# Kernel optimization log

Hardware: AMD Instinct MI355X
Metric: run time of the kernel (lower is better)

Reference implementation:

```python
import jax, jax.numpy as jnp
import numpy as np
from jax import lax

L = 12  # db6 filter length
REC_LO = np.array([0.11154074335008017, 0.4946238903983854, 0.7511339080215775,
                   0.3152503517092432, -0.22626469396516913, -0.12976686756709563,
                   0.09750160558707936, 0.02752286553001629, -0.031582039318031156,
                   0.0005538422009938016, 0.004777257511010651, -0.00107730108499558])
DEC_LO = REC_LO[::-1]
_sgn = (-1.0) ** np.arange(L)
DEC_HI = -_sgn * REC_LO            # pywt dec_hi
REC_HI = _sgn * DEC_LO             # pywt rec_hi
# XLA conv = cross-correlation; pytorch_wavelets correlates with reversed dec filters
K_ANA = np.ascontiguousarray(np.stack([DEC_LO[::-1], DEC_HI[::-1]])[:, None, :])  # (2,1,12)
# conv_transpose(stride2, pad L-2) == dilate-by-2, pad 1, correlate with flipped rec filters
K_SYN = np.ascontiguousarray(np.stack([REC_LO[::-1], REC_HI[::-1]])[None, :, :])  # (1,2,12)
J = 8


def _afb(x):
    # one analysis level, symmetric mode (pytorch_wavelets afb1d)
    B, C, N = x.shape
    out = (N + L - 1) // 2
    p = 2 * (out - 1) - N + L
    xp = jnp.pad(x, ((0, 0), (0, 0), (p // 2, p - p // 2)), mode='symmetric')
    y = lax.conv_general_dilated(xp.reshape(B * C, 1, -1), jnp.asarray(K_ANA, x.dtype),
                                 (2,), 'VALID', dimension_numbers=('NCH', 'OIH', 'NCH'))
    y = y.reshape(B, C, 2, out)
    return y[:, :, 0], y[:, :, 1]


def _sfb(lo, hi):
    # one synthesis level (pytorch_wavelets sfb1d); crop lo to hi length first
    lo = lo[..., :hi.shape[-1]]
    B, C, N = lo.shape
    z = jnp.stack([lo, hi], 2).reshape(B * C, 2, N)
    y = lax.conv_general_dilated(z, jnp.asarray(K_SYN, lo.dtype), (1,), [(1, 1)],
                                 lhs_dilation=(2,), dimension_numbers=('NCH', 'OIH', 'NCH'))
    return y.reshape(B, C, -1)  # length 2N - L + 2


def _wave_conv(x, w1, w2):
    lo, highs = x, []
    for _ in range(J):
        lo, hi = _afb(lo)
        highs.append(hi)
    lo = jnp.einsum('bix,iox->box', lo, w1)
    highs[-1] = jnp.einsum('bix,iox->box', highs[-1], w2)
    for hi in highs[::-1]:
        lo = _sfb(lo, hi)
    return lo


def _branch(xg, fc0_w, fc0_b, ww1, ww2, cw, cb, fc1_w, fc1_b, fc2_w, fc2_b):
    v = jnp.transpose(xg @ fc0_w + fc0_b, (0, 2, 1))  # (B,C,S)
    for i in range(4):
        a = _wave_conv(v, ww1[i], ww2[i])
        b = jnp.einsum('bcs,oc->bos', v, cw[i]) + cb[i][None, :, None]
        v = a + b
        if i < 3:
            v = jax.nn.gelu(v, approximate=False)
    v = jnp.transpose(v, (0, 2, 1))
    v = jax.nn.gelu(v @ fc1_w + fc1_b, approximate=False)
    return v @ fc2_w + fc2_b


def setup_inputs() -> dict:
    key = jax.random.key(0)
    ks = iter(jax.random.split(key, 32))
    B, S, W, LV = 64, 1024, 64, 8
    d = {"x": jax.random.normal(next(ks), (B, S, 1), jnp.float32)}
    def params(pref):
        sc = 1.0 / (W * W)
        d[pref + "fc0_w"] = jax.random.normal(next(ks), (2, W), jnp.float32) * 0.5
        d[pref + "fc0_b"] = jax.random.normal(next(ks), (W,), jnp.float32) * 0.1
        d[pref + "wave_w1"] = sc * jax.random.uniform(next(ks), (4, W, W, LV + 6), jnp.float32)
        d[pref + "wave_w2"] = sc * jax.random.uniform(next(ks), (4, W, W, LV + 6), jnp.float32)
        d[pref + "cw"] = jax.random.normal(next(ks), (4, W, W), jnp.float32) * (1.0 / np.sqrt(W))
        d[pref + "cb"] = jax.random.normal(next(ks), (4, W), jnp.float32) * 0.05
        d[pref + "fc1_w"] = jax.random.normal(next(ks), (W, 128), jnp.float32) * (1.0 / np.sqrt(W))
        d[pref + "fc1_b"] = jax.random.normal(next(ks), (128,), jnp.float32) * 0.05
        d[pref + "fc2_w"] = jax.random.normal(next(ks), (128, 1), jnp.float32) * (1.0 / np.sqrt(128))
        d[pref + "fc2_b"] = jax.random.normal(next(ks), (1,), jnp.float32) * 0.05
    params("")
    params("nt_")
    return d


def reference(x, fc0_w, fc0_b, wave_w1, wave_w2, cw, cb, fc1_w, fc1_b, fc2_w, fc2_b,
              nt_fc0_w, nt_fc0_b, nt_wave_w1, nt_wave_w2, nt_cw, nt_cb,
              nt_fc1_w, nt_fc1_b, nt_fc2_w, nt_fc2_b):
    B, S, _ = x.shape
    grid = jnp.broadcast_to(jnp.linspace(0.0, 1.0, S, dtype=x.dtype)[None, :, None], (B, S, 1))
    xg = jnp.concatenate([x, grid], -1)
    y = _branch(xg, fc0_w, fc0_b, wave_w1, wave_w2, cw, cb, fc1_w, fc1_b, fc2_w, fc2_b)
    y_nt = _branch(xg, nt_fc0_w, nt_fc0_b, nt_wave_w1, nt_wave_w2, nt_cw, nt_cb,
                   nt_fc1_w, nt_fc1_b, nt_fc2_w, nt_fc2_b)
    return y + y_nt
```

## Files before the change

kernel.cpp:

```cpp
#include <hip/hip_runtime.h>
#include <hip/hip_bf16.h>
#include <math.h>


#define BDIM 64
#define SLEN 1024
#define WCH  64
#define BC   (BDIM*WCH)
#define NT   16

typedef short s16x8 __attribute__((ext_vector_type(8)));
typedef float f32x4 __attribute__((ext_vector_type(4)));
typedef unsigned short u16x4 __attribute__((ext_vector_type(4)));

constexpr float RLv[12] = {
    0.11154074335008017f, 0.4946238903983854f, 0.7511339080215775f,
    0.3152503517092432f, -0.22626469396516913f, -0.12976686756709563f,
    0.09750160558707936f, 0.02752286553001629f, -0.031582039318031156f,
    0.0005538422009938016f, 0.004777257511010651f, -0.00107730108499558f };
constexpr float AHv[12] = {
     RLv[11], -RLv[10],  RLv[9], -RLv[8],  RLv[7], -RLv[6],
     RLv[5],  -RLv[4],   RLv[3], -RLv[2],  RLv[1], -RLv[0] };
constexpr float SLv[12] = {
     RLv[11], RLv[10], RLv[9], RLv[8], RLv[7], RLv[6],
     RLv[5],  RLv[4],  RLv[3], RLv[2], RLv[1], RLv[0] };
constexpr float SHv[12] = {
    -RLv[0],  RLv[1], -RLv[2],  RLv[3], -RLv[4],  RLv[5],
    -RLv[6],  RLv[7], -RLv[8],  RLv[9], -RLv[10], RLv[11] };

__device__ __forceinline__ float gelu_f(float x) {
    float z = 0.7978845608f * (x + 0.044715f * x * x * x);
    return x / (1.0f + __expf(-2.0f * z));
}
__device__ __forceinline__ unsigned short f2bf(float f) {
    __hip_bfloat16 h = __float2bfloat16(f);
    union { __hip_bfloat16 h; unsigned short u; } cv; cv.h = h; return cv.u;
}
__device__ __forceinline__ float bf2f(unsigned short u) {
    union { unsigned short u; __hip_bfloat16 h; } cv; cv.u = u;
    return __bfloat162float(cv.h);
}
__device__ __forceinline__ void unpack_frag2(uint4 a, uint4 b,
                                             s16x8* ah, s16x8* al) {
    union { s16x8 v; unsigned int d[4]; } H, L;
    H.d[0] = __builtin_amdgcn_perm(a.y, a.x, 0x05040100u);
    H.d[1] = __builtin_amdgcn_perm(a.w, a.z, 0x05040100u);
    H.d[2] = __builtin_amdgcn_perm(b.y, b.x, 0x05040100u);
    H.d[3] = __builtin_amdgcn_perm(b.w, b.z, 0x05040100u);
    L.d[0] = __builtin_amdgcn_perm(a.y, a.x, 0x07060302u);
    L.d[1] = __builtin_amdgcn_perm(a.w, a.z, 0x07060302u);
    L.d[2] = __builtin_amdgcn_perm(b.y, b.x, 0x07060302u);
    L.d[3] = __builtin_amdgcn_perm(b.w, b.z, 0x07060302u);
    *ah = H.v; *al = L.v;
}

__device__ __forceinline__ int swz(int c, int s) {
    return c * 64 + ((((s >> 3) ^ (c & 7)) << 3) | (s & 7));
}
__device__ __forceinline__ int swz2(int s, int c) {
    return s * 64 + ((((c >> 3) ^ (s & 7)) << 3) | (c & 7));
}

__device__ __forceinline__ void proj2(
    const unsigned short* Phi, const unsigned short* Plo,
    const unsigned short* __restrict__ Ahi, const unsigned short* __restrict__ Alo,
    float* __restrict__ Ppart, int bb, int tile, int s0, int t)
{
    const int lane = t & 63;
    const int w    = t >> 6;
    const int qr   = lane >> 4;
    const int ln   = lane & 15;

    s16x8 pah[2][2], pal[2][2];
#pragma unroll
    for (int kk = 0; kk < 2; ++kk)
#pragma unroll
        for (int mt = 0; mt < 2; ++mt) {
            const int arow = (mt * 16 + ln) * SLEN + s0 + kk * 32 + qr * 8;
            pah[kk][mt] = *(const s16x8*)&Ahi[arow];
            pal[kk][mt] = *(const s16x8*)&Alo[arow];
        }

    f32x4 pP[2][2], pS[2][2];
#pragma unroll
    for (int mt = 0; mt < 2; ++mt)
#pragma unroll
        for (int ni = 0; ni < 2; ++ni) {
            pP[mt][ni] = (f32x4){0.f,0.f,0.f,0.f};
            pS[mt][ni] = (f32x4){0.f,0.f,0.f,0.f};
        }

#pragma unroll
    for (int kk = 0; kk < 2; ++kk) {
        const int bk = kk * 4 + qr;
#pragma unroll
        for (int ni = 0; ni < 2; ++ni) {
            const int c = w * 32 + ni * 16 + ln;
            const int boff = c * 64 + ((bk ^ (c & 7)) << 3);
            s16x8 bh = *(const s16x8*)&Phi[boff];
            s16x8 bl = *(const s16x8*)&Plo[boff];
#pragma unroll
            for (int mt = 0; mt < 2; ++mt) {
                pP[mt][ni] = __builtin_amdgcn_mfma_f32_16x16x32_bf16(pah[kk][mt], bh, pP[mt][ni], 0, 0, 0);
                pS[mt][ni] = __builtin_amdgcn_mfma_f32_16x16x32_bf16(pal[kk][mt], bh, pS[mt][ni], 0, 0, 0);
                pS[mt][ni] = __builtin_amdgcn_mfma_f32_16x16x32_bf16(pah[kk][mt], bl, pS[mt][ni], 0, 0, 0);
            }
        }
    }
#pragma unroll
    for (int mt = 0; mt < 2; ++mt)
#pragma unroll
        for (int ni = 0; ni < 2; ++ni) {
            const int c = w * 32 + ni * 16 + ln;
            f32x4 pv = pP[mt][ni] + pS[mt][ni];
#pragma unroll
            for (int r = 0; r < 4; ++r) {
                const int xr = mt * 16 + qr * 4 + r;
                if (xr < 28)
                    Ppart[((size_t)(bb * NT + tile) * 28 + xr) * 64 + c] = pv[r];
            }
        }
}

__global__ __launch_bounds__(256) void setup_kernel(
    const float* __restrict__ x,
    unsigned short* __restrict__ Ahi, unsigned short* __restrict__ Alo,
    unsigned short* __restrict__ MThi, unsigned short* __restrict__ MTlo,
    float* __restrict__ axbuf,
    const float* __restrict__ fc1w_0, const float* __restrict__ fc1w_1,
    const float* __restrict__ cw_0, const float* __restrict__ cw_1,
    const float* __restrict__ w1_0, const float* __restrict__ w2_0,
    const float* __restrict__ w1_1, const float* __restrict__ w2_1,
    unsigned short* __restrict__ w1hi, unsigned short* __restrict__ w1lo,
    unsigned short* __restrict__ cwPhi, unsigned short* __restrict__ cwPlo,
    unsigned short* __restrict__ Dhi,  unsigned short* __restrict__ Dlo,
    float* __restrict__ WsT)
{
    __shared__ float Af[1024];
    __shared__ float Bff[520];
    __shared__ float hib[14];
    const int t = threadIdx.x;

    if (blockIdx.x < 1024 || (blockIdx.x >= 1052 && blockIdx.x < 1118)) {
        const bool isA = (blockIdx.x < 1024);
        const int s0 = blockIdx.x;
        const int di = blockIdx.x - 1052;
        for (int i = t; i < SLEN; i += 256) {
            float v;
            if (isA)           v = (i == s0) ? 1.0f : 0.0f;
            else if (di < 64)  v = x[di * SLEN + i];
            else if (di == 64) v = (float)i * (1.0f / 1023.0f);
            else               v = 1.0f;
            Af[i] = v;
        }
        __syncthreads();

        const int NIN[8]  = {1024, 517, 264, 137, 74, 42, 26, 18};
        const int NOUT[8] = { 517, 264, 137,  74, 42, 26, 18, 14};
#pragma unroll
        for (int lev = 0; lev < 8; ++lev) {
            float* in  = (lev & 1) ? Bff : Af;
            float* out = (lev & 1) ? Af : Bff;
            const int nin = NIN[lev], nout = NOUT[lev];
            for (int m = t; m < nout; m += 256) {
                float alo = 0.f, ahi = 0.f;
#pragma unroll
                for (int tt = 0; tt < 12; ++tt) {
                    int jj = 2 * m + tt - 10;
                    if (jj < 0)         jj = -1 - jj;
                    else if (jj >= nin) jj = 2 * nin - 1 - jj;
                    float xv = in[jj];
                    alo += xv * RLv[tt];
                    if (lev == 7) ahi += xv * AHv[tt];
                }
                out[m] = alo;
                if (lev == 7) {
                    if (isA) {
                        unsigned short h1 = f2bf(alo);
                        Ahi[m * SLEN + s0] = h1;
                        Alo[m * SLEN + s0] = f2bf(alo - bf2f(h1));
                        unsigned short h2 = f2bf(ahi);
                        Ahi[(14 + m) * SLEN + s0] = h2;
                        Alo[(14 + m) * SLEN + s0] = f2bf(ahi - bf2f(h2));
                    } else {
                        axbuf[di * 28 + m]      = alo;
                        axbuf[di * 28 + 14 + m] = ahi;
                    }
                }
            }
            __syncthreads();
        }
        if (isA && t < 4) {
            Ahi[(28 + t) * SLEN + s0] = 0; Alo[(28 + t) * SLEN + s0] = 0;
            MThi[s0 * 32 + 28 + t] = 0;    MTlo[s0 * 32 + 28 + t] = 0;
        }
        return;
    }

    if (blockIdx.x >= 1126) {
        const int wsb = blockIdx.x - 1126;
        const int L = wsb >> 2, br = (wsb >> 1) & 1, which = wsb & 1;
        const float* src = (which ? (br ? w2_1 : w2_0) : (br ? w1_1 : w1_0))
                         + (size_t)L * 64 * 64 * 14;
        const size_t dbase = ((size_t)(L * 2 + br) * 28 + which * 14) * 4096;
        for (int e = t; e < 4096; e += 256) {
            const float* sp = src + (size_t)e * 14;
            float v[14];
#pragma unroll
            for (int xi = 0; xi < 14; ++xi) v[xi] = sp[xi];
#pragma unroll
            for (int xi = 0; xi < 14; ++xi)
                WsT[dbase + (size_t)xi * 4096 + e] = v[xi];
        }
        return;
    }

    if (blockIdx.x >= 1118) {
        const int gid = (blockIdx.x - 1118) * 256 + t;
        for (int idx = gid; idx < 16384; idx += 2048) {
            int br = idx >> 13, r = idx & 8191;
            int h = r >> 6, c = r & 63;
            float f = (br ? fc1w_1 : fc1w_0)[c * 128 + h];
            unsigned short hh = f2bf(f);
            w1hi[idx] = hh;
            w1lo[idx] = f2bf(f - bf2f(hh));
        }
        for (int idx = gid; idx < 32768; idx += 2048) {
            int L = idx >> 13, br = (idx >> 12) & 1, e = idx & 4095;
            int k = e >> 6, o = e & 63;
            float val = (br ? cw_1 : cw_0)[(size_t)L * 4096 + o * 64 + k]
                      + ((k == o) ? 1.0f : 0.0f);
            unsigned short h = f2bf(val);
            const int off = (L * 2 + br) * 4096 + o * 64 + k;
            cwPhi[off] = h;
            cwPlo[off] = f2bf(val - bf2f(h));
        }
        for (int idx = gid; idx < 32768; idx += 2048) {
            int bb = idx >> 8, o = (idx >> 2) & 63, j = idx & 3;
            Dhi[bb * 2048 + o * 32 + 28 + j] = 0;
            Dlo[bb * 2048 + o * 32 + 28 + j] = 0;
        }
        return;
    }

    const int u = blockIdx.x - 1024;
    if (t < 14) {
        Af[t]  = (u < 14 && t == u) ? 1.0f : 0.0f;
        hib[t] = (u >= 14 && t == (u - 14)) ? 1.0f : 0.0f;
    }
    __syncthreads();

    const int NH[8] = {14, 18, 26, 42, 74, 137, 264, 517};
    const int NO[8] = {18, 26, 42, 74, 138, 264, 518, 1024};

#pragma unroll
    for (int s = 0; s < 8; ++s) {
        const float* lo = (s & 1) ? Bff : Af;
        float* out      = (s & 1) ? Af : Bff;
        const int N = NH[s], nout = NO[s];
        for (int m = t; m < nout; m += 256) {
            float acc = 0.f;
#pragma unroll
            for (int tt = 0; tt < 12; ++tt) {
                int uu = m + tt - 1;
                if ((uu & 1) == 0) {
                    int q = uu >> 1;
                    if (q < N) {
                        acc += lo[q] * SLv[tt];
                        if (s == 0) acc += hib[q] * SHv[tt];
                    }
                }
            }
            out[m] = acc;
        }
        __syncthreads();
    }
    for (int m = t; m < SLEN; m += 256) {
        float f = Af[m];
        unsigned short h = f2bf(f);
        MThi[m * 32 + u] = h;
        MTlo[m * 32 + u] = f2bf(f - bf2f(h));
    }
}

__global__ __launch_bounds__(256) void mix0_kernel(
    const float* __restrict__ axbuf,
    const float* __restrict__ fc0w_0, const float* __restrict__ fc0b_0,
    const float* __restrict__ fc0w_1, const float* __restrict__ fc0b_1,
    const float* __restrict__ WsT0,
    unsigned short* __restrict__ Dhi, unsigned short* __restrict__ Dlo)
{
    const int t = threadIdx.x;
    const int br  = blockIdx.x / 224;
    const int sub = blockIdx.x % 224;

    __shared__ float Ws[64][65];
    __shared__ float LO[8][64];
    const int o = t & 63;
    const int w = t >> 6;
    const int x  = sub >> 3;
    const int b0 = (sub & 7) << 3;

    const float* wsrc = WsT0 + ((size_t)(br * 28 + x)) * 4096;
    for (int idx = t; idx < 4096; idx += 256)
        Ws[idx >> 6][idx & 63] = wsrc[idx];

    const float* fc0w = br ? fc0w_1 : fc0w_0;
    const float* fc0b = br ? fc0b_1 : fc0b_0;
    const float agv = axbuf[64 * 28 + x];
    const float a1v = axbuf[65 * 28 + x];
    const float w0o = fc0w[o];
    const float wgo = fc0w[WCH + o];
    const float b0o = fc0b[o];

#pragma unroll
    for (int j = 0; j < 2; ++j) {
        int bi = w + 4 * j;
        int b  = b0 + bi;
        float axv = axbuf[b * 28 + x];
        LO[bi][o] = axv * w0o + agv * wgo + a1v * b0o;
    }
    __syncthreads();

#pragma unroll
    for (int j = 0; j < 2; ++j) {
        int bi = w + 4 * j;
        int bb = br * 64 + b0 + bi;
        float acc = 0.f;
        for (int i = 0; i < 64; ++i)
            acc += LO[bi][i] * Ws[i][o];
        acc -= LO[bi][o];
        unsigned short h = f2bf(acc);
        Dhi[bb * 2048 + o * 32 + x] = h;
        Dlo[bb * 2048 + o * 32 + x] = f2bf(acc - bf2f(h));
    }
}

__global__ __launch_bounds__(256) void mix_kernel(
    const float* __restrict__ Ppart,
    const float* __restrict__ WsTL,
    unsigned short* __restrict__ Dhi, unsigned short* __restrict__ Dlo)
{
    const int t = threadIdx.x;
    const int br  = blockIdx.x / 224;
    const int sub = blockIdx.x % 224;

    __shared__ float Ws[64][65];
    __shared__ float LO[8][64];
    const int o = t & 63;
    const int w = t >> 6;
    const int x  = sub >> 3;
    const int b0 = (sub & 7) << 3;

    const float* wsrc = WsTL + ((size_t)(br * 28 + x)) * 4096;
    for (int idx = t; idx < 4096; idx += 256)
        Ws[idx >> 6][idx & 63] = wsrc[idx];

#pragma unroll
    for (int j = 0; j < 2; ++j) {
        int bi = w + 4 * j;
        int bb = br * 64 + b0 + bi;
        float s = 0.f;
        for (int tile = 0; tile < NT; ++tile)
            s += Ppart[((size_t)(bb * NT + tile) * 28 + x) * 64 + o];
        LO[bi][o] = s;
    }
    __syncthreads();

#pragma unroll
    for (int j = 0; j < 2; ++j) {
        int bi = w + 4 * j;
        int bb = br * 64 + b0 + bi;
        float acc = 0.f;
        for (int i = 0; i < 64; ++i)
            acc += LO[bi][i] * Ws[i][o];
        acc -= LO[bi][o];
        unsigned short h = f2bf(acc);
        Dhi[bb * 2048 + o * 32 + x] = h;
        Dlo[bb * 2048 + o * 32 + x] = f2bf(acc - bf2f(h));
    }
}

__global__ __launch_bounds__(128, 3) void layer_kernel(
    const unsigned int* __restrict__ vin0, const unsigned int* __restrict__ vin1,
    unsigned int* __restrict__ vout0, unsigned int* __restrict__ vout1,
    const unsigned short* __restrict__ MThi, const unsigned short* __restrict__ MTlo,
    const unsigned short* __restrict__ Ahi,  const unsigned short* __restrict__ Alo,
    const unsigned short* __restrict__ cwPhi, const unsigned short* __restrict__ cwPlo,
    const unsigned short* __restrict__ Dhi,   const unsigned short* __restrict__ Dlo,
    const float* __restrict__ cb_0, const float* __restrict__ cb_1,
    const float* __restrict__ fc0w_0, const float* __restrict__ fc0b_0,
    const float* __restrict__ fc0w_1, const float* __restrict__ fc0b_1,
    const float* __restrict__ xin,
    float* __restrict__ Ppart, int Lidx)
{
    __shared__ unsigned short Phi[4096];
    __shared__ unsigned short Plo[4096];

    const int t = threadIdx.x;
    const int bid = blockIdx.x;
    const int br  = bid >> 10;
    const int rem = bid & 1023;
    const int b    = rem >> 4;
    const int tile = rem & 15;
    const int s0   = tile << 6;
    const size_t bS = (size_t)b * SLEN;
    const unsigned int* vin = br ? vin1 : vin0;
    unsigned int* vout      = br ? vout1 : vout0;
    const float* cb = br ? cb_1 : cb_0;
    const float* f0w = br ? fc0w_1 : fc0w_0;
    const float* f0b = br ? fc0b_1 : fc0b_0;
    const int bb = br * 64 + b;
    const int cwbase = (Lidx * 2 + br) * 4096;

    const int lane = t & 63;
    const int w    = t >> 6;
    const int qr   = lane >> 4;
    const int ln   = lane & 15;

    s16x8 Bh[2][2], Bl[2][2];
#pragma unroll
    for (int kk = 0; kk < 2; ++kk)
#pragma unroll
        for (int ni = 0; ni < 2; ++ni) {
            const int o = w * 32 + ni * 16 + ln;
            const int boff = cwbase + o * 64 + kk * 32 + qr * 8;
            Bh[kk][ni] = *(const s16x8*)&cwPhi[boff];
            Bl[kk][ni] = *(const s16x8*)&cwPlo[boff];
        }
    s16x8 Dhf[2], Dlf[2];
#pragma unroll
    for (int ni = 0; ni < 2; ++ni) {
        const int o = w * 32 + ni * 16 + ln;
        const int boff = bb * 2048 + o * 32 + qr * 8;
        Dhf[ni] = *(const s16x8*)&Dhi[boff];
        Dlf[ni] = *(const s16x8*)&Dlo[boff];
    }
    float cbv[2];
#pragma unroll
    for (int ni = 0; ni < 2; ++ni) cbv[ni] = cb[w * 32 + ni * 16 + ln];

    uint4 vb[2][2];
    float xpf = 0.f;
    if (Lidx == 0) {
        xpf = xin[bS + s0 + ln];
    } else {
        const size_t a0 = (bS + s0 + ln) * 64 + qr * 8;
        vb[0][0] = *(const uint4*)&vin[a0];
        vb[0][1] = *(const uint4*)&vin[a0 + 4];
        vb[1][0] = *(const uint4*)&vin[a0 + 32];
        vb[1][1] = *(const uint4*)&vin[a0 + 36];
    }

#pragma unroll
    for (int mi = 0; mi < 4; ++mi) {
        const int srow = mi * 16 + ln;
        uint4 vn[2][2];
        float xnf = 0.f;
        if (mi < 3) {
            if (Lidx == 0) {
                xnf = xin[bS + s0 + (mi + 1) * 16 + ln];
            } else {
                const size_t an = (bS + s0 + (mi + 1) * 16 + ln) * 64 + qr * 8;
                vn[0][0] = *(const uint4*)&vin[an];
                vn[0][1] = *(const uint4*)&vin[an + 4];
                vn[1][0] = *(const uint4*)&vin[an + 32];
                vn[1][1] = *(const uint4*)&vin[an + 36];
            }
        }

        f32x4 accP[2], accS[2];
#pragma unroll
        for (int ni = 0; ni < 2; ++ni) {
            accP[ni] = (f32x4){0.f,0.f,0.f,0.f};
            accS[ni] = (f32x4){0.f,0.f,0.f,0.f};
        }

#pragma unroll
        for (int kk = 0; kk < 2; ++kk) {
            s16x8 ah, al;
            if (Lidx == 0) {
                const int s = s0 + srow;
                const float gv = (float)s * (1.0f / 1023.0f);
#pragma unroll
                for (int j = 0; j < 8; ++j) {
                    const int c = kk * 32 + qr * 8 + j;
                    float val = xpf * f0w[c] + gv * f0w[WCH + c] + f0b[c];
                    unsigned short h = f2bf(val);
                    ah[j] = (short)h;
                    al[j] = (short)f2bf(val - bf2f(h));
                }
            } else {
                unpack_frag2(vb[kk][0], vb[kk][1], &ah, &al);
            }
#pragma unroll
            for (int ni = 0; ni < 2; ++ni) {
                accP[ni] = __builtin_amdgcn_mfma_f32_16x16x32_bf16(ah, Bh[kk][ni], accP[ni], 0, 0, 0);
                accS[ni] = __builtin_amdgcn_mfma_f32_16x16x32_bf16(al, Bh[kk][ni], accS[ni], 0, 0, 0);
                accS[ni] = __builtin_amdgcn_mfma_f32_16x16x32_bf16(ah, Bl[kk][ni], accS[ni], 0, 0, 0);
            }
        }
        {
            const size_t aoff = (size_t)(s0 + srow) * 32 + qr * 8;
            s16x8 mh = *(const s16x8*)&MThi[aoff];
            s16x8 ml = *(const s16x8*)&MTlo[aoff];
#pragma unroll
            for (int ni = 0; ni < 2; ++ni) {
                accP[ni] = __builtin_amdgcn_mfma_f32_16x16x32_bf16(mh, Dhf[ni], accP[ni], 0, 0, 0);
                accS[ni] = __builtin_amdgcn_mfma_f32_16x16x32_bf16(ml, Dhf[ni], accS[ni], 0, 0, 0);
                accS[ni] = __builtin_amdgcn_mfma_f32_16x16x32_bf16(mh, Dlf[ni], accS[ni], 0, 0, 0);
            }
        }
#pragma unroll
        for (int ni = 0; ni < 2; ++ni) {
            const int o = w * 32 + ni * 16 + ln;
            f32x4 acc = accP[ni] + accS[ni];
            u16x4 hv, lv;
#pragma unroll
            for (int r = 0; r < 4; ++r) {
                const int sl64 = mi * 16 + qr * 4 + r;
                float val = gelu_f(acc[r] + cbv[ni]);
                unsigned short h = f2bf(val);
                unsigned short l = f2bf(val - bf2f(h));
                vout[(bS + s0 + sl64) * 64 + o] =
                    (unsigned int)h | ((unsigned int)l << 16);
                hv[r] = h;
                lv[r] = l;
            }
            const int a = swz(o, mi * 16 + qr * 4);
            *(u16x4*)&Phi[a] = hv;
            *(u16x4*)&Plo[a] = lv;
        }
        if (mi < 3) {
            if (Lidx == 0) {
                xpf = xnf;
            } else {
                vb[0][0] = vn[0][0]; vb[0][1] = vn[0][1];
                vb[1][0] = vn[1][0]; vb[1][1] = vn[1][1];
            }
        }
    }

    proj2(Phi, Plo, Ahi, Alo, Ppart, bb, tile, s0, t);
}

__global__ __launch_bounds__(256, 2) void head_kernel(
    const unsigned int* __restrict__ vin0, const unsigned int* __restrict__ vin1,
    const unsigned short* __restrict__ MThi, const unsigned short* __restrict__ MTlo,
    const unsigned short* __restrict__ cwPhi, const unsigned short* __restrict__ cwPlo,
    const unsigned short* __restrict__ Dhi,   const unsigned short* __restrict__ Dlo,
    const float* __restrict__ cb_0, const float* __restrict__ cb_1,
    const unsigned short* __restrict__ w1hi, const unsigned short* __restrict__ w1lo,
    const float* __restrict__ fc1b_0, const float* __restrict__ fc2w_0,
    const float* __restrict__ fc2b_0,
    const float* __restrict__ fc1b_1, const float* __restrict__ fc2w_1,
    const float* __restrict__ fc2b_1,
    float* __restrict__ out)
{
    __shared__ unsigned short Vh[4096];
    __shared__ unsigned short Vl[4096];
    __shared__ float SP[4][32];

    const int t = threadIdx.x;
    const int bid = blockIdx.x;
    const int b    = bid >> 5;
    const int t32  = bid & 31;
    const int s0   = t32 << 5;
    const size_t bS = (size_t)b * SLEN;

    const int lane = t & 63;
    const int w    = t >> 6;
    const int br   = w >> 1;
    const int half = w & 1;
    const int qr   = lane >> 4;
    const int ln   = lane & 15;

    const unsigned int* vin = br ? vin1 : vin0;
    const float* cb   = (br ? cb_1 : cb_0) + 3 * WCH;
    const float* fc1b = br ? fc1b_1 : fc1b_0;
    const float* fc2w = br ? fc2w_1 : fc2w_0;
    const int bb = br * 64 + b;
    const int cwbase = (3 * 2 + br) * 4096;
    unsigned short* Vhp = Vh + br * 2048;
    unsigned short* Vlp = Vl + br * 2048;

    {
        s16x8 Bh[2][2], Bl[2][2];
#pragma unroll
        for (int kk = 0; kk < 2; ++kk)
#pragma unroll
            for (int ni = 0; ni < 2; ++ni) {
                const int o = half * 32 + ni * 16 + ln;
                const int boff = cwbase + o * 64 + kk * 32 + qr * 8;
                Bh[kk][ni] = *(const s16x8*)&cwPhi[boff];
                Bl[kk][ni] = *(const s16x8*)&cwPlo[boff];
            }
        s16x8 Dhf[2], Dlf[2];
#pragma unroll
        for (int ni = 0; ni < 2; ++ni) {
            const int o = half * 32 + ni * 16 + ln;
            const int boff = bb * 2048 + o * 32 + qr * 8;
            Dhf[ni] = *(const s16x8*)&Dhi[boff];
            Dlf[ni] = *(const s16x8*)&Dlo[boff];
        }
        float cbv[2];
#pragma unroll
        for (int ni = 0; ni < 2; ++ni) cbv[ni] = cb[half * 32 + ni * 16 + ln];

        uint4 vb[2][2];
        {
            const size_t a0 = (bS + s0 + ln) * 64 + qr * 8;
            vb[0][0] = *(const uint4*)&vin[a0];
            vb[0][1] = *(const uint4*)&vin[a0 + 4];
            vb[1][0] = *(const uint4*)&vin[a0 + 32];
            vb[1][1] = *(const uint4*)&vin[a0 + 36];
        }

#pragma unroll
        for (int mi = 0; mi < 2; ++mi) {
            uint4 vn[2][2];
            if (mi < 1) {
                const size_t an = (bS + s0 + 16 + ln) * 64 + qr * 8;
                vn[0][0] = *(const uint4*)&vin[an];
                vn[0][1] = *(const uint4*)&vin[an + 4];
                vn[1][0] = *(const uint4*)&vin[an + 32];
                vn[1][1] = *(const uint4*)&vin[an + 36];
            }
            const int srow = mi * 16 + ln;
            f32x4 accP[2], accS[2];
#pragma unroll
            for (int ni = 0; ni < 2; ++ni) {
                accP[ni] = (f32x4){0.f,0.f,0.f,0.f};
                accS[ni] = (f32x4){0.f,0.f,0.f,0.f};
            }

#pragma unroll
            for (int kk = 0; kk < 2; ++kk) {
                s16x8 ah, al;
                unpack_frag2(vb[kk][0], vb[kk][1], &ah, &al);
#pragma unroll
                for (int ni = 0; ni < 2; ++ni) {
                    accP[ni] = __builtin_amdgcn_mfma_f32_16x16x32_bf16(ah, Bh[kk][ni], accP[ni], 0, 0, 0);
                    accS[ni] = __builtin_amdgcn_mfma_f32_16x16x32_bf16(al, Bh[kk][ni], accS[ni], 0, 0, 0);
                    accS[ni] = __builtin_amdgcn_mfma_f32_16x16x32_bf16(ah, Bl[kk][ni], accS[ni], 0, 0, 0);
                }
            }
            {
                const size_t aoff = (size_t)(s0 + srow) * 32 + qr * 8;
                s16x8 mh = *(const s16x8*)&MThi[aoff];
                s16x8 ml = *(const s16x8*)&MTlo[aoff];
#pragma unroll
                for (int ni = 0; ni < 2; ++ni) {
                    accP[ni] = __builtin_amdgcn_mfma_f32_16x16x32_bf16(mh, Dhf[ni], accP[ni], 0, 0, 0);
                    accS[ni] = __builtin_amdgcn_mfma_f32_16x16x32_bf16(ml, Dhf[ni], accS[ni], 0, 0, 0);
                    accS[ni] = __builtin_amdgcn_mfma_f32_16x16x32_bf16(mh, Dlf[ni], accS[ni], 0, 0, 0);
                }
            }
#pragma unroll
            for (int ni = 0; ni < 2; ++ni) {
                const int o = half * 32 + ni * 16 + ln;
                f32x4 acc = accP[ni] + accS[ni];
#pragma unroll
                for (int r = 0; r < 4; ++r) {
                    const int sl32 = mi * 16 + qr * 4 + r;
                    float val = acc[r] + cbv[ni];
                    unsigned short h = f2bf(val);
                    unsigned short l = f2bf(val - bf2f(h));
                    const int a = swz2(sl32, o);
                    Vhp[a] = h;
                    Vlp[a] = l;
                }
            }
            if (mi < 1) {
                vb[0][0] = vn[0][0]; vb[0][1] = vn[0][1];
                vb[1][0] = vn[1][0]; vb[1][1] = vn[1][1];
            }
        }
    }
    __syncthreads();

    s16x8 Wh[2][4], Wl[2][4];
#pragma unroll
    for (int kk = 0; kk < 2; ++kk)
#pragma unroll
        for (int ni = 0; ni < 4; ++ni) {
            const int h = half * 64 + ni * 16 + ln;
            const int boff = br * 8192 + h * 64 + kk * 32 + qr * 8;
            Wh[kk][ni] = *(const s16x8*)&w1hi[boff];
            Wl[kk][ni] = *(const s16x8*)&w1lo[boff];
        }
    float b1v[4], w2v[4];
#pragma unroll
    for (int ni = 0; ni < 4; ++ni) {
        b1v[ni] = fc1b[half * 64 + ni * 16 + ln];
        w2v[ni] = fc2w[half * 64 + ni * 16 + ln];
    }

#pragma unroll
    for (int mi = 0; mi < 2; ++mi) {
        f32x4 a1P[4], a1S[4];
#pragma unroll
        for (int ni = 0; ni < 4; ++ni) {
            a1P[ni] = (f32x4){0.f,0.f,0.f,0.f};
            a1S[ni] = (f32x4){0.f,0.f,0.f,0.f};
        }

#pragma unroll
        for (int kk = 0; kk < 2; ++kk) {
            const int blk = kk * 4 + qr;
            const int sl  = mi * 16 + ln;
            const int a   = sl * 64 + ((blk ^ (sl & 7)) << 3);
            s16x8 ah = *(const s16x8*)&Vhp[a];
            s16x8 al = *(const s16x8*)&Vlp[a];
#pragma unroll
            for (int ni = 0; ni < 4; ++ni) {
                a1P[ni] = __builtin_amdgcn_mfma_f32_16x16x32_bf16(ah, Wh[kk][ni], a1P[ni], 0, 0, 0);
                a1S[ni] = __builtin_amdgcn_mfma_f32_16x16x32_bf16(al, Wh[kk][ni], a1S[ni], 0, 0, 0);
                a1S[ni] = __builtin_amdgcn_mfma_f32_16x16x32_bf16(ah, Wl[kk][ni], a1S[ni], 0, 0, 0);
            }
        }
        float partial[4] = {0.f, 0.f, 0.f, 0.f};
#pragma unroll
        for (int ni = 0; ni < 4; ++ni) {
            f32x4 acc1 = a1P[ni] + a1S[ni];
#pragma unroll
            for (int r = 0; r < 4; ++r)
                partial[r] += gelu_f(acc1[r] + b1v[ni]) * w2v[ni];
        }
#pragma unroll
        for (int r = 0; r < 4; ++r) {
            partial[r] += __shfl_xor(partial[r], 1, 64);
            partial[r] += __shfl_xor(partial[r], 2, 64);
            partial[r] += __shfl_xor(partial[r], 4, 64);
            partial[r] += __shfl_xor(partial[r], 8, 64);
        }
        if (ln == 0) {
#pragma unroll
            for (int r = 0; r < 4; ++r)
                SP[w][mi * 16 + qr * 4 + r] = partial[r];
        }
    }
    __syncthreads();

    if (t < 32) {
        const float bias = fc2b_0[0] + fc2b_1[0];
        out[bS + s0 + t] = SP[0][t] + SP[1][t] + SP[2][t] + SP[3][t] + bias;
    }
}

extern "C" void kernel_launch(void* const* d_in, const int* in_sizes, int n_in,
                              void* d_out, int out_size, void* d_ws, size_t ws_size,
                              hipStream_t stream)
{
    const float* x = (const float*)d_in[0];
    const float* P[2][10];
    for (int br = 0; br < 2; ++br)
        for (int k = 0; k < 10; ++k)
            P[br][k] = (const float*)d_in[1 + br * 10 + k];

    char* p = (char*)d_ws;
    const size_t PL = (size_t)BC * SLEN * 4;
    unsigned int* vplane[4];
    for (int i = 0; i < 4; ++i) { vplane[i] = (unsigned int*)p; p += PL; }
    unsigned short* Ahi  = (unsigned short*)p; p += 32 * SLEN * 2;
    unsigned short* Alo  = (unsigned short*)p; p += 32 * SLEN * 2;
    unsigned short* MThi = (unsigned short*)p; p += SLEN * 32 * 2;
    unsigned short* MTlo = (unsigned short*)p; p += SLEN * 32 * 2;
    float* Ppart = (float*)p;                  p += (size_t)128 * NT * 28 * 64 * 4;
    unsigned short* cwPhi = (unsigned short*)p; p += 8 * 4096 * 2;
    unsigned short* cwPlo = (unsigned short*)p; p += 8 * 4096 * 2;
    unsigned short* Dhi   = (unsigned short*)p; p += (size_t)128 * 2048 * 2;
    unsigned short* Dlo   = (unsigned short*)p; p += (size_t)128 * 2048 * 2;
    unsigned short* w1hi  = (unsigned short*)p; p += 2 * 8192 * 2;
    unsigned short* w1lo  = (unsigned short*)p; p += 2 * 8192 * 2;
    float* axbuf          = (float*)p;          p += 66 * 28 * 4;
    float* WsT            = (float*)p;          p += (size_t)4 * 2 * 28 * 4096 * 4;

    unsigned int *v0a = vplane[0], *v0b = vplane[1];
    unsigned int *v1a = vplane[2], *v1b = vplane[3];

    setup_kernel<<<1142, 256, 0, stream>>>(
        x, Ahi, Alo, MThi, MTlo, axbuf,
        P[0][6], P[1][6], P[0][4], P[1][4],
        P[0][2], P[0][3], P[1][2], P[1][3],
        w1hi, w1lo, cwPhi, cwPlo, Dhi, Dlo, WsT);

    mix0_kernel<<<448, 256, 0, stream>>>(
        axbuf, P[0][0], P[0][1], P[1][0], P[1][1],
        WsT, Dhi, Dlo);

    for (int i = 0; i < 3; ++i) {
        layer_kernel<<<2048, 128, 0, stream>>>(
            v0a, v1a, v0b, v1b,
            MThi, MTlo, Ahi, Alo, cwPhi, cwPlo, Dhi, Dlo,
            P[0][5] + (size_t)i * WCH, P[1][5] + (size_t)i * WCH,
            P[0][0], P[0][1], P[1][0], P[1][1], x,
            Ppart, i);
        unsigned int* tmp;
        tmp = v0a; v0a = v0b; v0b = tmp;
        tmp = v1a; v1a = v1b; v1b = tmp;

        mix_kernel<<<448, 256, 0, stream>>>(
            Ppart,
            WsT + (size_t)(i + 1) * 2 * 28 * 4096,
            Dhi, Dlo);
    }

    head_kernel<<<2048, 256, 0, stream>>>(
        v0a, v1a,
        MThi, MTlo, cwPhi, cwPlo, Dhi, Dlo,
        P[0][5] + (size_t)3 * WCH, P[1][5] + (size_t)3 * WCH,
        w1hi, w1lo,
        P[0][7], P[0][8], P[0][9],
        P[1][7], P[1][8], P[1][9],
        (float*)d_out);
}
```

Baseline: 262.7 us.

## Pre-swizzle MFMA operand buffers into fragment-major layout for contiguous loads

Setup, mix0 and mix kernels now write the bf16 hi/lo operand tables (A projection, MT transform, conv weights, D mixing, fc1 weights) directly in per-lane MFMA fragment order. The consuming layer and head kernels can then load each 8-element fragment as one contiguous 16-byte chunk per lane, so a wave reads a fully contiguous block instead of strided rows. This targets uncoalesced global loads of small constant operands in the hot kernels. The cost is scattered stores in the setup and mix kernels and more complex index math there.

Result: faster. 222.7 us (-15.2%).

```diff
diff --git a/kernel.cpp b/kernel.cpp
--- a/kernel.cpp
+++ b/kernel.cpp
@@ -61,10 +61,26 @@
     return s * 64 + ((((c >> 3) ^ (s & 7)) << 3) | (c & 7));
 }
 
+__device__ __host__ __forceinline__ int AF_IDX(int tile, int kk, int mt, int lane) {
+    return (((tile * 2 + kk) * 2 + mt) * 64 + lane) * 8;
+}
+__device__ __host__ __forceinline__ int MTF_IDX(int row16, int lane) {
+    return (row16 * 64 + lane) * 8;
+}
+__device__ __host__ __forceinline__ int CWF_IDX(int L, int br, int w, int kk, int ni) {
+    return ((((L * 2 + br) * 2 + w) * 2 + kk) * 2 + ni) * 512;
+}
+__device__ __host__ __forceinline__ int DF_IDX(int bb, int w, int ni) {
+    return ((bb * 2 + w) * 2 + ni) * 512;
+}
+__device__ __host__ __forceinline__ int W1F_IDX(int br, int half, int kk, int ni) {
+    return (((br * 2 + half) * 2 + kk) * 4 + ni) * 512;
+}
+
 __device__ __forceinline__ void proj2(
     const unsigned short* Phi, const unsigned short* Plo,
-    const unsigned short* __restrict__ Ahi, const unsigned short* __restrict__ Alo,
-    float* __restrict__ Ppart, int bb, int tile, int s0, int t)
+    const unsigned short* __restrict__ AFhi, const unsigned short* __restrict__ AFlo,
+    float* __restrict__ Ppart, int bb, int tile, int t)
 {
     const int lane = t & 63;
     const int w    = t >> 6;
@@ -76,9 +92,9 @@
     for (int kk = 0; kk < 2; ++kk)
 #pragma unroll
         for (int mt = 0; mt < 2; ++mt) {
-            const int arow = (mt * 16 + ln) * SLEN + s0 + kk * 32 + qr * 8;
-            pah[kk][mt] = *(const s16x8*)&Ahi[arow];
-            pal[kk][mt] = *(const s16x8*)&Alo[arow];
+            const int off = AF_IDX(tile, kk, mt, lane);
+            pah[kk][mt] = *(const s16x8*)&AFhi[off];
+            pal[kk][mt] = *(const s16x8*)&AFlo[off];
         }
 
     f32x4 pP[2][2], pS[2][2];
@@ -124,16 +140,16 @@
 
 __global__ __launch_bounds__(256) void setup_kernel(
     const float* __restrict__ x,
-    unsigned short* __restrict__ Ahi, unsigned short* __restrict__ Alo,
-    unsigned short* __restrict__ MThi, unsigned short* __restrict__ MTlo,
+    unsigned short* __restrict__ AFhi, unsigned short* __restrict__ AFlo,
+    unsigned short* __restrict__ MTFhi, unsigned short* __restrict__ MTFlo,
     float* __restrict__ axbuf,
     const float* __restrict__ fc1w_0, const float* __restrict__ fc1w_1,
     const float* __restrict__ cw_0, const float* __restrict__ cw_1,
     const float* __restrict__ w1_0, const float* __restrict__ w2_0,
     const float* __restrict__ w1_1, const float* __restrict__ w2_1,
-    unsigned short* __restrict__ w1hi, unsigned short* __restrict__ w1lo,
-    unsigned short* __restrict__ cwPhi, unsigned short* __restrict__ cwPlo,
-    unsigned short* __restrict__ Dhi,  unsigned short* __restrict__ Dlo,
+    unsigned short* __restrict__ w1Fhi, unsigned short* __restrict__ w1Flo,
+    unsigned short* __restrict__ cwFhi, unsigned short* __restrict__ cwFlo,
+    unsigned short* __restrict__ DFhi,  unsigned short* __restrict__ DFlo,
     float* __restrict__ WsT)
 {
     __shared__ float Af[1024];
@@ -157,6 +173,8 @@
 
         const int NIN[8]  = {1024, 517, 264, 137, 74, 42, 26, 18};
         const int NOUT[8] = { 517, 264, 137,  74, 42, 26, 18, 14};
+        const int tile = s0 >> 6, kkc = (s0 >> 5) & 1, qrc = (s0 >> 3) & 3,
+                  jc = s0 & 7;
 #pragma unroll
         for (int lev = 0; lev < 8; ++lev) {
             float* in  = (lev & 1) ? Bff : Af;
@@ -177,11 +195,20 @@
                 if (lev == 7) {
                     if (isA) {
                         unsigned short h1 = f2bf(alo);
-                        Ahi[m * SLEN + s0] = h1;
-                        Alo[m * SLEN + s0] = f2bf(alo - bf2f(h1));
+                        unsigned short l1 = f2bf(alo - bf2f(h1));
+                        {
+                            const int lane = qrc * 16 + (m & 15);
+                            const int off = AF_IDX(tile, kkc, m >> 4, lane) + jc;
+                            AFhi[off] = h1; AFlo[off] = l1;
+                        }
                         unsigned short h2 = f2bf(ahi);
-                        Ahi[(14 + m) * SLEN + s0] = h2;
-                        Alo[(14 + m) * SLEN + s0] = f2bf(ahi - bf2f(h2));
+                        unsigned short l2 = f2bf(ahi - bf2f(h2));
+                        {
+                            const int row = 14 + m;
+                            const int lane = qrc * 16 + (row & 15);
+                            const int off = AF_IDX(tile, kkc, row >> 4, lane) + jc;
+                            AFhi[off] = h2; AFlo[off] = l2;
+                        }
                     } else {
                         axbuf[di * 28 + m]      = alo;
                         axbuf[di * 28 + 14 + m] = ahi;
@@ -191,8 +218,18 @@
             __syncthreads();
         }
         if (isA && t < 4) {
-            Ahi[(28 + t) * SLEN + s0] = 0; Alo[(28 + t) * SLEN + s0] = 0;
-            MThi[s0 * 32 + 28 + t] = 0;    MTlo[s0 * 32 + 28 + t] = 0;
+            {
+                const int row = 28 + t;
+                const int lane = qrc * 16 + (row & 15);
+                const int off = AF_IDX(tile, kkc, 1, lane) + jc;
+                AFhi[off] = 0; AFlo[off] = 0;
+            }
+            {
+                const int col = 28 + t;
+                const int lane = (col >> 3) * 16 + (s0 & 15);
+                const int off = MTF_IDX(s0 >> 4, lane) + (col & 7);
+                MTFhi[off] = 0; MTFlo[off] = 0;
+            }
         }
         return;
     }
@@ -222,8 +259,11 @@
             int h = r >> 6, c = r & 63;
             float f = (br ? fc1w_1 : fc1w_0)[c * 128 + h];
             unsigned short hh = f2bf(f);
-            w1hi[idx] = hh;
-            w1lo[idx] = f2bf(f - bf2f(hh));
+            const int half = (h >> 6) & 1, ni = (h >> 4) & 3, lnh = h & 15;
+            const int kk = c >> 5, qr = (c >> 3) & 3, j = c & 7;
+            const int off = W1F_IDX(br, half, kk, ni) + (qr * 16 + lnh) * 8 + j;
+            w1Fhi[off] = hh;
+            w1Flo[off] = f2bf(f - bf2f(hh));
         }
         for (int idx = gid; idx < 32768; idx += 2048) {
             int L = idx >> 13, br = (idx >> 12) & 1, e = idx & 4095;
@@ -231,14 +271,19 @@
             float val = (br ? cw_1 : cw_0)[(size_t)L * 4096 + o * 64 + k]
                       + ((k == o) ? 1.0f : 0.0f);
             unsigned short h = f2bf(val);
-            const int off = (L * 2 + br) * 4096 + o * 64 + k;
-            cwPhi[off] = h;
-            cwPlo[off] = f2bf(val - bf2f(h));
+            const int w = o >> 5, ni = (o >> 4) & 1, lno = o & 15;
+            const int kk = k >> 5, qr = (k >> 3) & 3, j = k & 7;
+            const int off = CWF_IDX(L, br, w, kk, ni) + (qr * 16 + lno) * 8 + j;
+            cwFhi[off] = h;
+            cwFlo[off] = f2bf(val - bf2f(h));
         }
         for (int idx = gid; idx < 32768; idx += 2048) {
-            int bb = idx >> 8, o = (idx >> 2) & 63, j = idx & 3;
-            Dhi[bb * 2048 + o * 32 + 28 + j] = 0;
-            Dlo[bb * 2048 + o * 32 + 28 + j] = 0;
+            int bb = idx >> 8, o = (idx >> 2) & 63, j3 = idx & 3;
+            const int x = 28 + j3;
+            const int w = o >> 5, ni = (o >> 4) & 1, lno = o & 15;
+            const int off = DF_IDX(bb, w, ni) + ((x >> 3) * 16 + lno) * 8 + (x & 7);
+            DFhi[off] = 0;
+            DFlo[off] = 0;
         }
         return;
     }
@@ -275,11 +320,15 @@
         }
         __syncthreads();
     }
-    for (int m = t; m < SLEN; m += 256) {
-        float f = Af[m];
-        unsigned short h = f2bf(f);
-        MThi[m * 32 + u] = h;
-        MTlo[m * 32 + u] = f2bf(f - bf2f(h));
+    {
+        const int qr = u >> 3, j = u & 7;
+        for (int m = t; m < SLEN; m += 256) {
+            float f = Af[m];
+            unsigned short h = f2bf(f);
+            const int off = MTF_IDX(m >> 4, qr * 16 + (m & 15)) + j;
+            MTFhi[off] = h;
+            MTFlo[off] = f2bf(f - bf2f(h));
+        }
     }
 }
 
@@ -288,7 +337,7 @@
     const float* __restrict__ fc0w_0, const float* __restrict__ fc0b_0,
     const float* __restrict__ fc0w_1, const float* __restrict__ fc0b_1,
     const float* __restrict__ WsT0,
-    unsigned short* __restrict__ Dhi, unsigned short* __restrict__ Dlo)
+    unsigned short* __restrict__ DFhi, unsigned short* __restrict__ DFlo)
 {
     const int t = threadIdx.x;
     const int br  = blockIdx.x / 224;
@@ -322,6 +371,8 @@
     }
     __syncthreads();
 
+    const int wo = o >> 5, nio = (o >> 4) & 1, lno = o & 15;
+    const int dsub = ((x >> 3) * 16 + lno) * 8 + (x & 7);
 #pragma unroll
     for (int j = 0; j < 2; ++j) {
         int bi = w + 4 * j;
@@ -331,15 +382,16 @@
             acc += LO[bi][i] * Ws[i][o];
         acc -= LO[bi][o];
         unsigned short h = f2bf(acc);
-        Dhi[bb * 2048 + o * 32 + x] = h;
-        Dlo[bb * 2048 + o * 32 + x] = f2bf(acc - bf2f(h));
+        const int off = DF_IDX(bb, wo, nio) + dsub;
+        DFhi[off] = h;
+        DFlo[off] = f2bf(acc - bf2f(h));
     }
 }
 
 __global__ __launch_bounds__(256) void mix_kernel(
     const float* __restrict__ Ppart,
     const float* __restrict__ WsTL,
-    unsigned short* __restrict__ Dhi, unsigned short* __restrict__ Dlo)
+    unsigned short* __restrict__ DFhi, unsigned short* __restrict__ DFlo)
 {
     const int t = threadIdx.x;
     const int br  = blockIdx.x / 224;
@@ -367,6 +419,8 @@
     }
     __syncthreads();
 
+    const int wo = o >> 5, nio = (o >> 4) & 1, lno = o & 15;
+    const int dsub = ((x >> 3) * 16 + lno) * 8 + (x & 7);
 #pragma unroll
     for (int j = 0; j < 2; ++j) {
         int bi = w + 4 * j;
@@ -376,18 +430,19 @@
             acc += LO[bi][i] * Ws[i][o];
         acc -= LO[bi][o];
         unsigned short h = f2bf(acc);
-        Dhi[bb * 2048 + o * 32 + x] = h;
-        Dlo[bb * 2048 + o * 32 + x] = f2bf(acc - bf2f(h));
+        const int off = DF_IDX(bb, wo, nio) + dsub;
+        DFhi[off] = h;
+        DFlo[off] = f2bf(acc - bf2f(h));
     }
 }
 
 __global__ __launch_bounds__(128, 3) void layer_kernel(
     const unsigned int* __restrict__ vin0, const unsigned int* __restrict__ vin1,
     unsigned int* __restrict__ vout0, unsigned int* __restrict__ vout1,
-    const unsigned short* __restrict__ MThi, const unsigned short* __restrict__ MTlo,
-    const unsigned short* __restrict__ Ahi,  const unsigned short* __restrict__ Alo,
-    const unsigned short* __restrict__ cwPhi, const unsigned short* __restrict__ cwPlo,
-    const unsigned short* __restrict__ Dhi,   const unsigned short* __restrict__ Dlo,
+    const unsigned short* __restrict__ MTFhi, const unsigned short* __restrict__ MTFlo,
+    const unsigned short* __restrict__ AFhi,  const unsigned short* __restrict__ AFlo,
+    const unsigned short* __restrict__ cwFhi, const unsigned short* __restrict__ cwFlo,
+    const unsigned short* __restrict__ DFhi,   const unsigned short* __restrict__ DFlo,
     const float* __restrict__ cb_0, const float* __restrict__ cb_1,
     const float* __restrict__ fc0w_0, const float* __restrict__ fc0b_0,
     const float* __restrict__ fc0w_1, const float* __restrict__ fc0b_1,
@@ -411,7 +466,6 @@
     const float* f0w = br ? fc0w_1 : fc0w_0;
     const float* f0b = br ? fc0b_1 : fc0b_0;
     const int bb = br * 64 + b;
-    const int cwbase = (Lidx * 2 + br) * 4096;
 
     const int lane = t & 63;
     const int w    = t >> 6;
@@ -423,18 +477,16 @@
     for (int kk = 0; kk < 2; ++kk)
 #pragma unroll
         for (int ni = 0; ni < 2; ++ni) {
-            const int o = w * 32 + ni * 16 + ln;
-            const int boff = cwbase + o * 64 + kk * 32 + qr * 8;
-            Bh[kk][ni] = *(const s16x8*)&cwPhi[boff];
-            Bl[kk][ni] = *(const s16x8*)&cwPlo[boff];
+            const int off = CWF_IDX(Lidx, br, w, kk, ni) + lane * 8;
+            Bh[kk][ni] = *(const s16x8*)&cwFhi[off];
+            Bl[kk][ni] = *(const s16x8*)&cwFlo[off];
         }
     s16x8 Dhf[2], Dlf[2];
 #pragma unroll
     for (int ni = 0; ni < 2; ++ni) {
-        const int o = w * 32 + ni * 16 + ln;
-        const int boff = bb * 2048 + o * 32 + qr * 8;
-        Dhf[ni] = *(const s16x8*)&Dhi[boff];
-        Dlf[ni] = *(const s16x8*)&Dlo[boff];
+        const int off = DF_IDX(bb, w, ni) + lane * 8;
+        Dhf[ni] = *(const s16x8*)&DFhi[off];
+        Dlf[ni] = *(const s16x8*)&DFlo[off];
     }
     float cbv[2];
 #pragma unroll
@@ -501,9 +553,9 @@
             }
         }
         {
-            const size_t aoff = (size_t)(s0 + srow) * 32 + qr * 8;
-            s16x8 mh = *(const s16x8*)&MThi[aoff];
-            s16x8 ml = *(const s16x8*)&MTlo[aoff];
+            const int off = MTF_IDX((s0 >> 4) + mi, lane);
+            s16x8 mh = *(const s16x8*)&MTFhi[off];
+            s16x8 ml = *(const s16x8*)&MTFlo[off];
 #pragma unroll
             for (int ni = 0; ni < 2; ++ni) {
                 accP[ni] = __builtin_amdgcn_mfma_f32_16x16x32_bf16(mh, Dhf[ni], accP[ni], 0, 0, 0);
@@ -541,16 +593,16 @@
         }
     }
 
-    proj2(Phi, Plo, Ahi, Alo, Ppart, bb, tile, s0, t);
+    proj2(Phi, Plo, AFhi, AFlo, Ppart, bb, tile, t);
 }
 
 __global__ __launch_bounds__(256, 2) void head_kernel(
     const unsigned int* __restrict__ vin0, const unsigned int* __restrict__ vin1,
-    const unsigned short* __restrict__ MThi, const unsigned short* __restrict__ MTlo,
-    const unsigned short* __restrict__ cwPhi, const unsigned short* __restrict__ cwPlo,
-    const unsigned short* __restrict__ Dhi,   const unsigned short* __restrict__ Dlo,
+    const unsigned short* __restrict__ MTFhi, const unsigned short* __restrict__ MTFlo,
+    const unsigned short* __restrict__ cwFhi, const unsigned short* __restrict__ cwFlo,
+    const unsigned short* __restrict__ DFhi,   const unsigned short* __restrict__ DFlo,
     const float* __restrict__ cb_0, const float* __restrict__ cb_1,
-    const unsigned short* __restrict__ w1hi, const unsigned short* __restrict__ w1lo,
+    const unsigned short* __restrict__ w1Fhi, const unsigned short* __restrict__ w1Flo,
     const float* __restrict__ fc1b_0, const float* __restrict__ fc2w_0,
     const float* __restrict__ fc2b_0,
     const float* __restrict__ fc1b_1, const float* __restrict__ fc2w_1,
@@ -580,7 +632,6 @@
     const float* fc1b = br ? fc1b_1 : fc1b_0;
     const float* fc2w = br ? fc2w_1 : fc2w_0;
     const int bb = br * 64 + b;
-    const int cwbase = (3 * 2 + br) * 4096;
     unsigned short* Vhp = Vh + br * 2048;
     unsigned short* Vlp = Vl + br * 2048;
 
@@ -590,18 +641,16 @@
         for (int kk = 0; kk < 2; ++kk)
 #pragma unroll
             for (int ni = 0; ni < 2; ++ni) {
-                const int o = half * 32 + ni * 16 + ln;
-                const int boff = cwbase + o * 64 + kk * 32 + qr * 8;
-                Bh[kk][ni] = *(const s16x8*)&cwPhi[boff];
-                Bl[kk][ni] = *(const s16x8*)&cwPlo[boff];
+                const int off = CWF_IDX(3, br, half, kk, ni) + lane * 8;
+                Bh[kk][ni] = *(const s16x8*)&cwFhi[off];
+                Bl[kk][ni] = *(const s16x8*)&cwFlo[off];
             }
         s16x8 Dhf[2], Dlf[2];
 #pragma unroll
         for (int ni = 0; ni < 2; ++ni) {
-            const int o = half * 32 + ni * 16 + ln;
-            const int boff = bb * 2048 + o * 32 + qr * 8;
-            Dhf[ni] = *(const s16x8*)&Dhi[boff];
-            Dlf[ni] = *(const s16x8*)&Dlo[boff];
+            const int off = DF_IDX(bb, half, ni) + lane * 8;
+            Dhf[ni] = *(const s16x8*)&DFhi[off];
+            Dlf[ni] = *(const s16x8*)&DFlo[off];
         }
         float cbv[2];
 #pragma unroll
@@ -626,7 +675,6 @@
                 vn[1][0] = *(const uint4*)&vin[an + 32];
                 vn[1][1] = *(const uint4*)&vin[an + 36];
             }
-            const int srow = mi * 16 + ln;
             f32x4 accP[2], accS[2];
 #pragma unroll
             for (int ni = 0; ni < 2; ++ni) {
@@ -646,9 +694,9 @@
                 }
             }
             {
-                const size_t aoff = (size_t)(s0 + srow) * 32 + qr * 8;
-                s16x8 mh = *(const s16x8*)&MThi[aoff];
-                s16x8 ml = *(const s16x8*)&MTlo[aoff];
+                const int off = MTF_IDX(t32 * 2 + mi, lane);
+                s16x8 mh = *(const s16x8*)&MTFhi[off];
+                s16x8 ml = *(const s16x8*)&MTFlo[off];
 #pragma unroll
                 for (int ni = 0; ni < 2; ++ni) {
                     accP[ni] = __builtin_amdgcn_mfma_f32_16x16x32_bf16(mh, Dhf[ni], accP[ni], 0, 0, 0);
@@ -684,10 +732,9 @@
     for (int kk = 0; kk < 2; ++kk)
 #pragma unroll
         for (int ni = 0; ni < 4; ++ni) {
-            const int h = half * 64 + ni * 16 + ln;
-            const int boff = br * 8192 + h * 64 + kk * 32 + qr * 8;
-            Wh[kk][ni] = *(const s16x8*)&w1hi[boff];
-            Wl[kk][ni] = *(const s16x8*)&w1lo[boff];
+            const int off = W1F_IDX(br, half, kk, ni) + lane * 8;
+            Wh[kk][ni] = *(const s16x8*)&w1Fhi[off];
+            Wl[kk][ni] = *(const s16x8*)&w1Flo[off];
         }
     float b1v[4], w2v[4];
 #pragma unroll
@@ -762,17 +809,17 @@
     const size_t PL = (size_t)BC * SLEN * 4;
     unsigned int* vplane[4];
     for (int i = 0; i < 4; ++i) { vplane[i] = (unsigned int*)p; p += PL; }
-    unsigned short* Ahi  = (unsigned short*)p; p += 32 * SLEN * 2;
-    unsigned short* Alo  = (unsigned short*)p; p += 32 * SLEN * 2;
-    unsigned short* MThi = (unsigned short*)p; p += SLEN * 32 * 2;
-    unsigned short* MTlo = (unsigned short*)p; p += SLEN * 32 * 2;
+    unsigned short* AFhi  = (unsigned short*)p; p += 32768 * 2;
+    unsigned short* AFlo  = (unsigned short*)p; p += 32768 * 2;
+    unsigned short* MTFhi = (unsigned short*)p; p += 32768 * 2;
+    unsigned short* MTFlo = (unsigned short*)p; p += 32768 * 2;
     float* Ppart = (float*)p;                  p += (size_t)128 * NT * 28 * 64 * 4;
-    unsigned short* cwPhi = (unsigned short*)p; p += 8 * 4096 * 2;
-    unsigned short* cwPlo = (unsigned short*)p; p += 8 * 4096 * 2;
-    unsigned short* Dhi   = (unsigned short*)p; p += (size_t)128 * 2048 * 2;
-    unsigned short* Dlo   = (unsigned short*)p; p += (size_t)128 * 2048 * 2;
-    unsigned short* w1hi  = (unsigned short*)p; p += 2 * 8192 * 2;
-    unsigned short* w1lo  = (unsigned short*)p; p += 2 * 8192 * 2;
+    unsigned short* cwFhi = (unsigned short*)p; p += 32768 * 2;
+    unsigned short* cwFlo = (unsigned short*)p; p += 32768 * 2;
+    unsigned short* DFhi  = (unsigned short*)p; p += (size_t)128 * 2048 * 2;
+    unsigned short* DFlo  = (unsigned short*)p; p += (size_t)128 * 2048 * 2;
+    unsigned short* w1Fhi = (unsigned short*)p; p += 16384 * 2;
+    unsigned short* w1Flo = (unsigned short*)p; p += 16384 * 2;
     float* axbuf          = (float*)p;          p += 66 * 28 * 4;
     float* WsT            = (float*)p;          p += (size_t)4 * 2 * 28 * 4096 * 4;
 
@@ -780,19 +827,19 @@
     unsigned int *v1a = vplane[2], *v1b = vplane[3];
 
     setup_kernel<<<1142, 256, 0, stream>>>(
-        x, Ahi, Alo, MThi, MTlo, axbuf,
+        x, AFhi, AFlo, MTFhi, MTFlo, axbuf,
         P[0][6], P[1][6], P[0][4], P[1][4],
         P[0][2], P[0][3], P[1][2], P[1][3],
-        w1hi, w1lo, cwPhi, cwPlo, Dhi, Dlo, WsT);
+        w1Fhi, w1Flo, cwFhi, cwFlo, DFhi, DFlo, WsT);
 
     mix0_kernel<<<448, 256, 0, stream>>>(
         axbuf, P[0][0], P[0][1], P[1][0], P[1][1],
-        WsT, Dhi, Dlo);
+        WsT, DFhi, DFlo);
 
     for (int i = 0; i < 3; ++i) {
         layer_kernel<<<2048, 128, 0, stream>>>(
             v0a, v1a, v0b, v1b,
-            MThi, MTlo, Ahi, Alo, cwPhi, cwPlo, Dhi, Dlo,
+            MTFhi, MTFlo, AFhi, AFlo, cwFhi, cwFlo, DFhi, DFlo,
             P[0][5] + (size_t)i * WCH, P[1][5] + (size_t)i * WCH,
             P[0][0], P[0][1], P[1][0], P[1][1], x,
             Ppart, i);
@@ -803,14 +850,14 @@
         mix_kernel<<<448, 256, 0, stream>>>(
             Ppart,
             WsT + (size_t)(i + 1) * 2 * 28 * 4096,
-            Dhi, Dlo);
+            DFhi, DFlo);
     }
 
     head_kernel<<<2048, 256, 0, stream>>>(
         v0a, v1a,
-        MThi, MTlo, cwPhi, cwPlo, Dhi, Dlo,
+        MTFhi, MTFlo, cwFhi, cwFlo, DFhi, DFlo,
         P[0][5] + (size_t)3 * WCH, P[1][5] + (size_t)3 * WCH,
-        w1hi, w1lo,
+        w1Fhi, w1Flo,
         P[0][7], P[0][8], P[0][9],
         P[1][7], P[1][8], P[1][9],
         (float*)d_out);
```
